# Kernel tuning notes

Hardware: AMD Instinct MI355X
Metric: run time of the kernel (lower is better)

The kernel has to match this reference:

```python
import jax, jax.numpy as jnp
import numpy as np

# ---- static config ----
B, H, W, C = 32, 64, 64, 256
WS, SHIFT, NH = 8, 4, 8
HD = C // NH
N = WS * WS  # tokens per window
NW = (H // WS) * (W // WS)
EPS = 1e-5


def _relative_position_index(ws):
    ch, cw = np.meshgrid(np.arange(ws), np.arange(ws), indexing='ij')
    coords = np.stack([ch, cw]).reshape(2, -1)          # (2, N)
    rel = coords[:, :, None] - coords[:, None, :]        # (2, N, N)
    rel = rel.transpose(1, 2, 0)
    rel[:, :, 0] += ws - 1
    rel[:, :, 1] += ws - 1
    rel[:, :, 0] *= 2 * ws - 1
    return jnp.asarray(rel.sum(-1))                      # (N, N) int


def _shifted_window_mask(h, w, ws, shift):
    img = np.zeros((h, w))
    slices = (slice(0, -ws), slice(-ws, -shift), slice(-shift, None))
    cnt = 0
    for hs in slices:
        for wsl in slices:
            img[hs, wsl] = cnt
            cnt += 1
    mw = img.reshape(h // ws, ws, w // ws, ws).transpose(0, 2, 1, 3).reshape(-1, ws * ws)
    diff = mw[:, None, :] - mw[:, :, None]
    return jnp.asarray(np.where(diff != 0, -100.0, 0.0).astype(np.float32))  # (nW, N, N)


REL_IDX = _relative_position_index(WS)
ATTN_MASK = _shifted_window_mask(H, W, WS, SHIFT)


def _layernorm(x, g, b):
    mu = jnp.mean(x, axis=-1, keepdims=True)
    var = jnp.mean(jnp.square(x - mu), axis=-1, keepdims=True)
    return (x - mu) * jax.lax.rsqrt(var + EPS) * g + b


def _window_partition(x):  # (B,H,W,C) -> (B*nW, N, C)
    x = x.reshape(B, H // WS, WS, W // WS, WS, C)
    return x.transpose(0, 1, 3, 2, 4, 5).reshape(-1, N, C)


def _window_reverse(win):  # (B*nW, N, C) -> (B,H,W,C)
    x = win.reshape(B, H // WS, W // WS, WS, WS, C)
    return x.transpose(0, 1, 3, 2, 4, 5).reshape(B, H, W, C)


def setup_inputs() -> dict:
    key = jax.random.key(0)
    ks = jax.random.split(key, 6)
    s = lambda fan_in: 1.0 / np.sqrt(fan_in)
    return {
        'x': jax.random.normal(ks[0], (B, H * W, C), jnp.float32),
        'norm1_g': jnp.ones((C,), jnp.float32),
        'norm1_b': jnp.zeros((C,), jnp.float32),
        'qkv_w': jax.random.normal(ks[1], (C, 3 * C), jnp.float32) * s(C),
        'qkv_b': jnp.zeros((3 * C,), jnp.float32),
        'proj_w': jax.random.normal(ks[2], (C, C), jnp.float32) * s(C),
        'proj_b': jnp.zeros((C,), jnp.float32),
        'bias_table': jax.random.normal(ks[3], ((2 * WS - 1) ** 2, NH), jnp.float32) * 0.02,
        'norm2_g': jnp.ones((C,), jnp.float32),
        'norm2_b': jnp.zeros((C,), jnp.float32),
        'fc1_w': jax.random.normal(ks[4], (C, 4 * C), jnp.float32) * s(C),
        'fc1_b': jnp.zeros((4 * C,), jnp.float32),
        'fc2_w': jax.random.normal(ks[5], (4 * C, C), jnp.float32) * s(4 * C),
        'fc2_b': jnp.zeros((C,), jnp.float32),
    }


def reference(x, norm1_g, norm1_b, qkv_w, qkv_b, proj_w, proj_b, bias_table,
              norm2_g, norm2_b, fc1_w, fc1_b, fc2_w, fc2_b):
    shortcut = x
    h = _layernorm(x, norm1_g, norm1_b).reshape(B, H, W, C)
    # cyclic shift
    h = jnp.roll(h, shift=(-SHIFT, -SHIFT), axis=(1, 2))
    xw = _window_partition(h)                               # (Bw, N, C), Bw = B*nW
    # window attention
    qkv = xw @ qkv_w + qkv_b                                 # (Bw, N, 3C)
    qkv = qkv.reshape(-1, N, 3, NH, HD).transpose(2, 0, 3, 1, 4)
    q, k, v = qkv[0], qkv[1], qkv[2]                         # (Bw, NH, N, HD)
    attn = jnp.einsum('whnd,whmd->whnm', q * (HD ** -0.5), k)
    rpb = bias_table[REL_IDX.reshape(-1)].reshape(N, N, NH).transpose(2, 0, 1)
    attn = attn + rpb[None]
    attn = attn.reshape(B, NW, NH, N, N) + ATTN_MASK[None, :, None]
    attn = jax.nn.softmax(attn.reshape(-1, NH, N, N), axis=-1)
    out = jnp.einsum('whnm,whmd->whnd', attn, v)
    out = out.transpose(0, 2, 1, 3).reshape(-1, N, C)
    out = out @ proj_w + proj_b
    # reverse windows + shift back
    h = _window_reverse(out)
    h = jnp.roll(h, shift=(SHIFT, SHIFT), axis=(1, 2)).reshape(B, H * W, C)
    x = shortcut + h
    # MLP with pre-norm residual
    m = _layernorm(x, norm2_g, norm2_b)
    m = jax.nn.gelu(m @ fc1_w + fc1_b, approximate=False) @ fc2_w + fc2_b
    return x + m
```

## Files before the change

### kernel.cpp

```cpp
#include <hip/hip_runtime.h>
#include <hip/hip_bf16.h>


typedef __bf16 bf16;
typedef __bf16 bf16x8 __attribute__((ext_vector_type(8)));
typedef __bf16 bf16x4 __attribute__((ext_vector_type(4)));
typedef float  f32x4  __attribute__((ext_vector_type(4)));

#define M_TOK 131072

#define GLDS(gp, lp)                                                                   \
    __builtin_amdgcn_global_load_lds(                                                  \
        (const __attribute__((address_space(1))) unsigned int*)(gp),                   \
        (__attribute__((address_space(3))) unsigned int*)(lp), 16, 0, 0)

__global__ __launch_bounds__(256) void prep_all(const float* __restrict__ qkv_w,
                                                const float* __restrict__ proj_w,
                                                const float* __restrict__ fc1_w,
                                                const float* __restrict__ fc2_w,
                                                const float* __restrict__ bt,
                                                bf16* __restrict__ WQ, bf16* __restrict__ WP,
                                                bf16* __restrict__ W1, bf16* __restrict__ W2,
                                                float* __restrict__ rpb) {
    int idx = blockIdx.x * 256 + threadIdx.x;
    if (idx < 196608) {
        int k = idx / 768, n = idx - k * 768;
        WQ[(size_t)n * 256 + k] = (bf16)qkv_w[idx];
    } else if (idx < 262144) {
        int l = idx - 196608;
        int k = l >> 8, n = l & 255;
        WP[(size_t)n * 256 + k] = (bf16)proj_w[l];
    } else if (idx < 524288) {
        int l = idx - 262144;
        int k = l >> 10, n = l & 1023;
        W1[(size_t)n * 256 + k] = (bf16)fc1_w[l];
    } else if (idx < 786432) {
        int l = idx - 524288;
        int k = l >> 8, n = l & 255;
        W2[(size_t)n * 1024 + k] = (bf16)fc2_w[l];
    } else {
        int l = idx - 786432;
        int h = l >> 12, n = (l >> 6) & 63, m = l & 63;
        int ridx = ((n >> 3) - (m >> 3) + 7) * 15 + ((n & 7) - (m & 7) + 7);
        rpb[l] = bt[ridx * 8 + h];
    }
}

__global__ __launch_bounds__(256) void ln_k(const float* __restrict__ x,
                                            const float* __restrict__ g,
                                            const float* __restrict__ bb,
                                            bf16* __restrict__ dst) {
    int t = blockIdx.x * 4 + (threadIdx.x >> 6);
    int lane = threadIdx.x & 63;
    int w = t >> 6, n = t & 63;
    int b = w >> 6, nw = w & 63;
    int r = ((nw >> 3) * 8 + (n >> 3) + 4) & 63;
    int c = ((nw & 7) * 8 + (n & 7) + 4) & 63;
    size_t src = ((size_t)b * 4096 + r * 64 + c) * 256;
    float4 v = *(const float4*)&x[src + lane * 4];
    float s = v.x + v.y + v.z + v.w;
    float sq = v.x * v.x + v.y * v.y + v.z * v.z + v.w * v.w;
#pragma unroll
    for (int off = 1; off < 64; off <<= 1) {
        s += __shfl_xor(s, off);
        sq += __shfl_xor(sq, off);
    }
    float mean = s * (1.0f / 256.0f);
    float var = sq * (1.0f / 256.0f) - mean * mean;
    float rstd = rsqrtf(var + 1e-5f);
    float4 gg = *(const float4*)&g[lane * 4];
    float4 bv = *(const float4*)&bb[lane * 4];
    bf16x4 o;
    o[0] = (bf16)((v.x - mean) * rstd * gg.x + bv.x);
    o[1] = (bf16)((v.y - mean) * rstd * gg.y + bv.y);
    o[2] = (bf16)((v.z - mean) * rstd * gg.z + bv.z);
    o[3] = (bf16)((v.w - mean) * rstd * gg.w + bv.w);
    *(bf16x4*)&dst[(size_t)t * 256 + lane * 4] = o;
}

__device__ __forceinline__ float fast_gelu(float v) {
    float t = v * v;
    float w = __builtin_fmaf(0.044715f * t, v, v);
    float e = __expf(-1.5957691216057308f * w);
    return v * __builtin_amdgcn_rcpf(1.0f + e);
}

template <int NDIM, int KDIM, int EPI>
__global__ __launch_bounds__(256) void gemm_k(const bf16* __restrict__ A,
                                              const bf16* __restrict__ Bt,
                                              const float* __restrict__ bias,
                                              bf16* __restrict__ outb,
                                              float* __restrict__ outf,
                                              const bf16* __restrict__ baseb) {
    __shared__ __align__(16) bf16 SH[24576];
    constexpr int NBN = NDIM / 128;
    constexpr int NK = KDIM / 32;
    const int tid = threadIdx.x;
    const int nwg = gridDim.x;
    const int flat = blockIdx.x;
    const int cpx = nwg >> 3;
    const int orig = (flat & 7) * cpx + (flat >> 3);
    const int bm = orig / NBN, bn = orig % NBN;

    const int lane = tid & 63, wid = tid >> 6;
    const int wr = wid >> 1, wc = wid & 1;
    const int lhi = lane >> 4, llo = lane & 15;

    f32x4 acc[4][4];
#pragma unroll
    for (int i = 0; i < 4; i++)
#pragma unroll
        for (int j = 0; j < 4; j++) acc[i][j] = f32x4{0.f, 0.f, 0.f, 0.f};

    const int srow = wid * 32 + (lane >> 2);
    const int scol = (((lane & 3) - ((lane >> 3) & 3)) & 3) * 8;
    const bf16* Ap = A + (size_t)(bm * 128 + srow) * KDIM + scol;
    const bf16* Bp = Bt + (size_t)(bn * 128 + srow) * KDIM + scol;
    const int gsw = ((lhi + (llo >> 1)) & 3) * 8;

#define STAGE(bufidx)                                                                  \
    do {                                                                               \
        bf16* Al = SH + (bufidx)*4096 + wid * 1024;                                    \
        bf16* Bl = SH + 12288 + (bufidx)*4096 + wid * 1024;                            \
        GLDS(Ap, Al);                                                                  \
        GLDS(Ap + 16 * KDIM, Al + 16 * 32);                                            \
        GLDS(Bp, Bl);                                                                  \
        GLDS(Bp + 16 * KDIM, Bl + 16 * 32);                                            \
        Ap += 32;                                                                      \
        Bp += 32;                                                                      \
    } while (0)

#define COMPUTE(bufidx)                                                                \
    do {                                                                               \
        const int ab = (bufidx)*4096;                                                  \
        bf16x8 af[4], bfr[4];                                                          \
        _Pragma("unroll") for (int mi = 0; mi < 4; mi++) af[mi] =                      \
            *(const bf16x8*)&SH[ab + (wr * 64 + mi * 16 + llo) * 32 + gsw];            \
        _Pragma("unroll") for (int ni = 0; ni < 4; ni++) bfr[ni] =                     \
            *(const bf16x8*)&SH[12288 + ab + (wc * 64 + ni * 16 + llo) * 32 + gsw];    \
        _Pragma("unroll") for (int mi = 0; mi < 4; mi++)                               \
            _Pragma("unroll") for (int ni = 0; ni < 4; ni++) acc[mi][ni] =             \
                __builtin_amdgcn_mfma_f32_16x16x32_bf16(bfr[ni], af[mi],               \
                                                        acc[mi][ni], 0, 0, 0);         \
    } while (0)

#define WAITBAR(N)                                                                     \
    asm volatile("s_waitcnt vmcnt(" #N ")" ::: "memory");                              \
    __builtin_amdgcn_s_barrier();                                                      \
    __builtin_amdgcn_sched_barrier(0)

#define END_PHASE                                                                      \
    asm volatile("s_waitcnt lgkmcnt(0)" ::: "memory");                                 \
    __builtin_amdgcn_s_barrier();                                                      \
    __builtin_amdgcn_sched_barrier(0)

    STAGE(0);
    STAGE(1);
    STAGE(2);
    int buf = 0;
    for (int i = 0; i + 3 < NK; ++i) {
        WAITBAR(8);
        COMPUTE(buf);
        END_PHASE;
        STAGE(buf);
        buf = (buf == 2) ? 0 : buf + 1;
    }
    WAITBAR(8);
    COMPUTE(buf);
    buf = (buf == 2) ? 0 : buf + 1;
    WAITBAR(4);
    COMPUTE(buf);
    buf = (buf == 2) ? 0 : buf + 1;
    WAITBAR(0);
    COMPUTE(buf);

#undef STAGE
#undef COMPUTE
#undef WAITBAR
#undef END_PHASE

    __syncthreads();

    char* shb = (char*)SH;
    if constexpr (EPI == 0 || EPI == 2) {
#pragma unroll
        for (int ni = 0; ni < 4; ni++) {
            const int lcol = wc * 64 + ni * 16 + lhi * 4;
            const float4 b4 = *(const float4*)&bias[bn * 128 + lcol];
#pragma unroll
            for (int mi = 0; mi < 4; mi++) {
                const int ltok = wr * 64 + mi * 16 + llo;
                float v0 = acc[mi][ni][0] + b4.x;
                float v1 = acc[mi][ni][1] + b4.y;
                float v2 = acc[mi][ni][2] + b4.z;
                float v3 = acc[mi][ni][3] + b4.w;
                bf16x4 o;
                if constexpr (EPI == 2) {
                    o[0] = (bf16)fast_gelu(v0); o[1] = (bf16)fast_gelu(v1);
                    o[2] = (bf16)fast_gelu(v2); o[3] = (bf16)fast_gelu(v3);
                } else {
                    o[0] = (bf16)v0; o[1] = (bf16)v1; o[2] = (bf16)v2; o[3] = (bf16)v3;
                }
                const int u2 = (lcol >> 3) ^ (ltok & 15);
                *(bf16x4*)(shb + ltok * 256 + u2 * 16 + (lcol & 7) * 2) = o;
            }
        }
        __syncthreads();
        const int j = lane & 15;
#pragma unroll
        for (int rnd = 0; rnd < 8; rnd++) {
            const int ltok = wid * 32 + rnd * 4 + (lane >> 4);
            const int u2 = j ^ (ltok & 15);
            bf16x8 v = *(const bf16x8*)(shb + ltok * 256 + u2 * 16);
            *(bf16x8*)&outb[(size_t)(bm * 128 + ltok) * NDIM + bn * 128 + j * 8] = v;
        }
    } else {
#pragma unroll
        for (int p = 0; p < 2; p++) {
            if (wc == p) {
#pragma unroll
                for (int ni = 0; ni < 4; ni++) {
                    const int lcolh = ni * 16 + lhi * 4;
                    const float4 b4 = *(const float4*)&bias[bn * 128 + p * 64 + lcolh];
#pragma unroll
                    for (int mi = 0; mi < 4; mi++) {
                        const int ltok = wr * 64 + mi * 16 + llo;
                        float4 o = {acc[mi][ni][0] + b4.x, acc[mi][ni][1] + b4.y,
                                    acc[mi][ni][2] + b4.z, acc[mi][ni][3] + b4.w};
                        const int u2 = (lcolh >> 2) ^ (ltok & 15);
                        *(float4*)(shb + ltok * 256 + u2 * 16) = o;
                    }
                }
            }
            __syncthreads();
            const int j = lane & 15;
#pragma unroll
            for (int rnd = 0; rnd < 8; rnd++) {
                const int ltok = wid * 32 + rnd * 4 + (lane >> 4);
                const int u2 = j ^ (ltok & 15);
                float4 v = *(const float4*)(shb + ltok * 256 + u2 * 16);
                const int gcol = bn * 128 + p * 64 + j * 4;
                const int grow = bm * 128 + ltok;
                size_t dst = (size_t)grow * NDIM + gcol;
                bf16x4 bb = *(const bf16x4*)&baseb[dst];
                float4 o = {v.x + (float)bb[0], v.y + (float)bb[1],
                            v.z + (float)bb[2], v.w + (float)bb[3]};
                *(float4*)&outf[dst] = o;
            }
            if (p == 0) __syncthreads();
        }
    }
}

__global__ __launch_bounds__(256) void proj_ln_k(const bf16* __restrict__ A,
                                                 const bf16* __restrict__ Bt,
                                                 const float* __restrict__ bias,
                                                 const float* __restrict__ resid,
                                                 bf16* __restrict__ baseb,
                                                 const float* __restrict__ g2,
                                                 const float* __restrict__ b2,
                                                 bf16* __restrict__ hb) {
    __shared__ __align__(16) bf16 SH[20480];
    constexpr int KDIM = 256;
    const int tid = threadIdx.x;
    const int nwg = gridDim.x;
    const int flat = blockIdx.x;
    const int cpx = nwg >> 3;
    const int bm = (flat & 7) * cpx + (flat >> 3);

    const int lane = tid & 63, wid = tid >> 6;
    const int lhi = lane >> 4, llo = lane & 15;

    f32x4 acc[4][4];
#pragma unroll
    for (int i = 0; i < 4; i++)
#pragma unroll
        for (int j = 0; j < 4; j++) acc[i][j] = f32x4{0.f, 0.f, 0.f, 0.f};

    const int scol = (((lane & 3) - ((lane >> 3) & 3)) & 3) * 8;
    const bf16* Ap = A + (size_t)(bm * 64 + wid * 16 + (lane >> 2)) * KDIM + scol;
    const bf16* Bp = Bt + (size_t)(wid * 64 + (lane >> 2)) * KDIM + scol;
    const int gsw = ((lhi + (llo >> 1)) & 3) * 8;

#define PSTAGE(bufidx)                                                                 \
    do {                                                                               \
        bf16* Al = SH + (bufidx)*2048 + wid * 512;                                     \
        bf16* Bl = SH + 4096 + (bufidx)*8192 + wid * 2048;                             \
        GLDS(Ap, Al);                                                                  \
        GLDS(Bp, Bl);                                                                  \
        GLDS(Bp + 16 * KDIM, Bl + 512);                                                \
        GLDS(Bp + 32 * KDIM, Bl + 1024);                                               \
        GLDS(Bp + 48 * KDIM, Bl + 1536);                                               \
        Ap += 32;                                                                      \
        Bp += 32;                                                                      \
    } while (0)

#define PCOMPUTE(bufidx)                                                               \
    do {                                                                               \
        bf16x8 af[4], bfr[4];                                                          \
        _Pragma("unroll") for (int mi = 0; mi < 4; mi++) af[mi] =                      \
            *(const bf16x8*)&SH[(bufidx)*2048 + (mi * 16 + llo) * 32 + gsw];           \
        _Pragma("unroll") for (int ni = 0; ni < 4; ni++) bfr[ni] =                     \
            *(const bf16x8*)&SH[4096 + (bufidx)*8192 +                                 \
                                (wid * 64 + ni * 16 + llo) * 32 + gsw];                \
        _Pragma("unroll") for (int mi = 0; mi < 4; mi++)                               \
            _Pragma("unroll") for (int ni = 0; ni < 4; ni++) acc[mi][ni] =             \
                __builtin_amdgcn_mfma_f32_16x16x32_bf16(bfr[ni], af[mi],               \
                                                        acc[mi][ni], 0, 0, 0);         \
    } while (0)

    PSTAGE(0);
    PSTAGE(1);
    int buf = 0;
    for (int i = 0; i + 2 < 8; ++i) {
        asm volatile("s_waitcnt vmcnt(5)" ::: "memory");
        __builtin_amdgcn_s_barrier();
        __builtin_amdgcn_sched_barrier(0);
        PCOMPUTE(buf);
        asm volatile("s_waitcnt lgkmcnt(0)" ::: "memory");
        __builtin_amdgcn_s_barrier();
        __builtin_amdgcn_sched_barrier(0);
        PSTAGE(buf);
        buf ^= 1;
    }
    asm volatile("s_waitcnt vmcnt(5)" ::: "memory");
    __builtin_amdgcn_s_barrier();
    __builtin_amdgcn_sched_barrier(0);
    PCOMPUTE(buf);
    buf ^= 1;
    asm volatile("s_waitcnt vmcnt(0)" ::: "memory");
    __builtin_amdgcn_s_barrier();
    __builtin_amdgcn_sched_barrier(0);
    PCOMPUTE(buf);

#undef PSTAGE
#undef PCOMPUTE

    char* shb = (char*)SH;
    const float4 gg = *(const float4*)&g2[lane * 4];
    const float4 bb4 = *(const float4*)&b2[lane * 4];
#pragma unroll
    for (int p = 0; p < 2; p++) {
        __syncthreads();
#pragma unroll
        for (int ni = 0; ni < 4; ni++) {
            const int col0 = wid * 64 + ni * 16 + lhi * 4;
            const float4 b4 = *(const float4*)&bias[col0];
#pragma unroll
            for (int m2 = 0; m2 < 2; m2++) {
                const int mi = 2 * p + m2;
                const int lt = m2 * 16 + llo;
                float4 o = {acc[mi][ni][0] + b4.x, acc[mi][ni][1] + b4.y,
                            acc[mi][ni][2] + b4.z, acc[mi][ni][3] + b4.w};
                const int u2 = (col0 >> 2) ^ (lt & 15);
                *(float4*)(shb + lt * 1024 + u2 * 16) = o;
            }
        }
        __syncthreads();
#pragma unroll
        for (int rnd = 0; rnd < 8; rnd++) {
            const int lt = rnd * 4 + wid;
            const int u2 = lane ^ (lt & 15);
            float4 v = *(const float4*)(shb + lt * 1024 + u2 * 16);
            const int grow = bm * 64 + p * 32 + lt;
            int w = grow >> 6, n = grow & 63;
            int b = w >> 6, nw = w & 63;
            int rr = ((nw >> 3) * 8 + (n >> 3) + 4) & 63;
            int cc = ((nw & 7) * 8 + (n & 7) + 4) & 63;
            const size_t rowbase = ((size_t)b * 4096 + rr * 64 + cc) * 256;
            float4 rs = *(const float4*)&resid[rowbase + lane * 4];
            float4 o = {rs.x + v.x, rs.y + v.y, rs.z + v.z, rs.w + v.w};
            bf16x4 bo = {(bf16)o.x, (bf16)o.y, (bf16)o.z, (bf16)o.w};
            *(bf16x4*)&baseb[rowbase + lane * 4] = bo;
            float s = o.x + o.y + o.z + o.w;
            float sq = o.x * o.x + o.y * o.y + o.z * o.z + o.w * o.w;
#pragma unroll
            for (int off = 1; off < 64; off <<= 1) {
                s += __shfl_xor(s, off);
                sq += __shfl_xor(sq, off);
            }
            float mean = s * (1.0f / 256.0f);
            float var = sq * (1.0f / 256.0f) - mean * mean;
            float rstd = rsqrtf(var + 1e-5f);
            bf16x4 ho;
            ho[0] = (bf16)((o.x - mean) * rstd * gg.x + bb4.x);
            ho[1] = (bf16)((o.y - mean) * rstd * gg.y + bb4.y);
            ho[2] = (bf16)((o.z - mean) * rstd * gg.z + bb4.z);
            ho[3] = (bf16)((o.w - mean) * rstd * gg.w + bb4.w);
            *(bf16x4*)&hb[rowbase + lane * 4] = ho;
        }
    }
}

__device__ __forceinline__ int regid3(int p) { return p < 56 ? 0 : (p < 60 ? 1 : 2); }

__global__ __launch_bounds__(256) void attn_k(const bf16* __restrict__ qkv,
                                              const float* __restrict__ rpb,
                                              bf16* __restrict__ aout) {
    __shared__ __align__(16) bf16 Pl[4][64 * 80];
    const int wid = threadIdx.x >> 6, lane = threadIdx.x & 63;
    const int lhi = lane >> 4, llo = lane & 15;
    const int wh = blockIdx.x * 4 + wid;
    const int w = wh >> 3, h = wh & 7;
    const bf16* base = qkv + (size_t)w * (64 * 768);

    bf16x8 qf[4], kf[4];
#pragma unroll
    for (int i = 0; i < 4; i++)
        qf[i] = *(const bf16x8*)(base + (i * 16 + llo) * 768 + h * 32 + lhi * 8);
#pragma unroll
    for (int i = 0; i < 4; i++)
        kf[i] = *(const bf16x8*)(base + (i * 16 + llo) * 768 + 256 + h * 32 + lhi * 8);
    f32x4 s[4][4];
#pragma unroll
    for (int mi = 0; mi < 4; mi++)
#pragma unroll
        for (int ni = 0; ni < 4; ni++) {
            s[mi][ni] = f32x4{0.f, 0.f, 0.f, 0.f};
            s[mi][ni] =
                __builtin_amdgcn_mfma_f32_16x16x32_bf16(qf[mi], kf[ni], s[mi][ni], 0, 0, 0);
        }

    const int nw = w & 63;
    const int pr0 = (nw >> 3) * 8, pc0 = (nw & 7) * 8;
    int creg[4];
#pragma unroll
    for (int ni = 0; ni < 4; ni++) {
        int m = ni * 16 + llo;
        creg[ni] = regid3(pr0 + (m >> 3)) * 3 + regid3(pc0 + (m & 7));
    }
    float rmax[4][4], rsum[4][4];
#pragma unroll
    for (int mi = 0; mi < 4; mi++)
#pragma unroll
        for (int r = 0; r < 4; r++) {
            int n = mi * 16 + lhi * 4 + r;
            int rreg = regid3(pr0 + (n >> 3)) * 3 + regid3(pc0 + (n & 7));
            float mx = -1e30f;
#pragma unroll
            for (int ni = 0; ni < 4; ni++) {
                int m = ni * 16 + llo;
                float sv = s[mi][ni][r] * 0.17677669529663687f + rpb[(h * 64 + n) * 64 + m] +
                           (rreg == creg[ni] ? 0.0f : -100.0f);
                s[mi][ni][r] = sv;
                mx = fmaxf(mx, sv);
            }
            rmax[mi][r] = mx;
        }
#pragma unroll
    for (int off = 1; off < 16; off <<= 1)
#pragma unroll
        for (int mi = 0; mi < 4; mi++)
#pragma unroll
            for (int r = 0; r < 4; r++)
                rmax[mi][r] = fmaxf(rmax[mi][r], __shfl_xor(rmax[mi][r], off));
#pragma unroll
    for (int mi = 0; mi < 4; mi++)
#pragma unroll
        for (int r = 0; r < 4; r++) {
            float a = 0.f;
#pragma unroll
            for (int ni = 0; ni < 4; ni++) {
                float p = __expf(s[mi][ni][r] - rmax[mi][r]);
                s[mi][ni][r] = p;
                a += p;
            }
            rsum[mi][r] = a;
        }
#pragma unroll
    for (int off = 1; off < 16; off <<= 1)
#pragma unroll
        for (int mi = 0; mi < 4; mi++)
#pragma unroll
            for (int r = 0; r < 4; r++) rsum[mi][r] += __shfl_xor(rsum[mi][r], off);

    bf16* P = Pl[wid];
#pragma unroll
    for (int mi = 0; mi < 4; mi++)
#pragma unroll
        for (int r = 0; r < 4; r++) {
            float rinv = 1.0f / rsum[mi][r];
            int row = mi * 16 + lhi * 4 + r;
#pragma unroll
            for (int ni = 0; ni < 4; ni++)
                P[row * 80 + ni * 16 + llo] = (bf16)(s[mi][ni][r] * rinv);
        }

    f32x4 o[4][2];
#pragma unroll
    for (int mi = 0; mi < 4; mi++)
#pragma unroll
        for (int ni = 0; ni < 2; ni++) o[mi][ni] = f32x4{0.f, 0.f, 0.f, 0.f};
#pragma unroll
    for (int kc = 0; kc < 2; kc++) {
        bf16x8 pf[4], vf[2];
#pragma unroll
        for (int mi = 0; mi < 4; mi++)
            pf[mi] = *(const bf16x8*)(P + (mi * 16 + llo) * 80 + kc * 32 + lhi * 8);
#pragma unroll
        for (int ni = 0; ni < 2; ni++)
#pragma unroll
            for (int j = 0; j < 8; j++)
                vf[ni][j] = base[(kc * 32 + lhi * 8 + j) * 768 + 512 + h * 32 + ni * 16 + llo];
#pragma unroll
        for (int mi = 0; mi < 4; mi++)
#pragma unroll
            for (int ni = 0; ni < 2; ni++)
                o[mi][ni] =
                    __builtin_amdgcn_mfma_f32_16x16x32_bf16(pf[mi], vf[ni], o[mi][ni], 0, 0, 0);
    }
#pragma unroll
    for (int mi = 0; mi < 4; mi++)
#pragma unroll
        for (int ni = 0; ni < 2; ni++)
#pragma unroll
            for (int r = 0; r < 4; r++) {
                int row = mi * 16 + lhi * 4 + r;
                aout[(size_t)(w * 64 + row) * 256 + h * 32 + ni * 16 + llo] =
                    (bf16)o[mi][ni][r];
            }
}

extern "C" void kernel_launch(void* const* d_in, const int* in_sizes, int n_in,
                              void* d_out, int out_size, void* d_ws, size_t ws_size,
                              hipStream_t stream) {
    const float* x      = (const float*)d_in[0];
    const float* n1g    = (const float*)d_in[1];
    const float* n1b    = (const float*)d_in[2];
    const float* qkv_w  = (const float*)d_in[3];
    const float* qkv_b  = (const float*)d_in[4];
    const float* proj_w = (const float*)d_in[5];
    const float* proj_b = (const float*)d_in[6];
    const float* btab   = (const float*)d_in[7];
    const float* n2g    = (const float*)d_in[8];
    const float* n2b    = (const float*)d_in[9];
    const float* fc1_w  = (const float*)d_in[10];
    const float* fc1_b  = (const float*)d_in[11];
    const float* fc2_w  = (const float*)d_in[12];
    const float* fc2_b  = (const float*)d_in[13];
    float* out = (float*)d_out;
    char* ws = (char*)d_ws;

    constexpr size_t MB = 1048576ull;
    bf16* XW    = (bf16*)(ws);
    bf16* BASEB = (bf16*)(ws);
    bf16* QKVB  = (bf16*)(ws + 67 * MB);
    bf16* Gbuf  = (bf16*)(ws + 67 * MB);
    bf16* Hb    = (bf16*)(ws + 201 * MB);
    bf16* ATTN  = (bf16*)(ws + 268 * MB);
    bf16* WQ    = (bf16*)(ws + 335 * MB);
    bf16* WP    = (bf16*)(ws + 335 * MB + 393216);
    bf16* W1    = (bf16*)(ws + 335 * MB + 524288);
    bf16* W2    = (bf16*)(ws + 335 * MB + 1048576);
    float* RPB  = (float*)(ws + 335 * MB + 1572864);

    dim3 blk(256);
    prep_all<<<3200, blk, 0, stream>>>(qkv_w, proj_w, fc1_w, fc2_w, btab,
                                       WQ, WP, W1, W2, RPB);

    ln_k<<<M_TOK / 4, blk, 0, stream>>>(x, n1g, n1b, XW);

    for (int c = 0; c < 2; ++c) {
        const size_t toff = (size_t)c * 65536;
        gemm_k<768, 256, 0><<<3072, blk, 0, stream>>>(XW + toff * 256, WQ, qkv_b,
                                                      QKVB, nullptr, nullptr);
        attn_k<<<2048, blk, 0, stream>>>(QKVB, RPB, ATTN + toff * 256);
    }

    proj_ln_k<<<2048, blk, 0, stream>>>(ATTN, WP, proj_b, x, BASEB, n2g, n2b, Hb);

    for (int q = 0; q < 2; ++q) {
        const size_t toff = (size_t)q * 65536;
        gemm_k<1024, 256, 2><<<4096, blk, 0, stream>>>(Hb + toff * 256, W1, fc1_b,
                                                       Gbuf, nullptr, nullptr);
        gemm_k<256, 1024, 3><<<1024, blk, 0, stream>>>(Gbuf, W2, fc2_b, nullptr,
                                                       out + toff * 256,
                                                       BASEB + toff * 256);
    }
}
```

Measured before the change: 584.4 us.

## Chunk whole block into four token slices and triple-buffer proj GEMM

```diff
diff --git a/kernel.cpp b/kernel.cpp
--- a/kernel.cpp
+++ b/kernel.cpp
@@ -6,8 +6,6 @@
 typedef __bf16 bf16x8 __attribute__((ext_vector_type(8)));
 typedef __bf16 bf16x4 __attribute__((ext_vector_type(4)));
 typedef float  f32x4  __attribute__((ext_vector_type(4)));
-
-#define M_TOK 131072
 
 #define GLDS(gp, lp)                                                                   \
     __builtin_amdgcn_global_load_lds(                                                  \
@@ -260,7 +258,7 @@
                                                  const float* __restrict__ g2,
                                                  const float* __restrict__ b2,
                                                  bf16* __restrict__ hb) {
-    __shared__ __align__(16) bf16 SH[20480];
+    __shared__ __align__(16) bf16 SH[32768];
     constexpr int KDIM = 256;
     const int tid = threadIdx.x;
     const int nwg = gridDim.x;
@@ -285,7 +283,7 @@
 #define PSTAGE(bufidx)                                                                 \
     do {                                                                               \
         bf16* Al = SH + (bufidx)*2048 + wid * 512;                                     \
-        bf16* Bl = SH + 4096 + (bufidx)*8192 + wid * 2048;                             \
+        bf16* Bl = SH + 6144 + (bufidx)*8192 + wid * 2048;                             \
         GLDS(Ap, Al);                                                                  \
         GLDS(Bp, Bl);                                                                  \
         GLDS(Bp + 16 * KDIM, Bl + 512);                                                \
@@ -301,7 +299,7 @@
         _Pragma("unroll") for (int mi = 0; mi < 4; mi++) af[mi] =                      \
             *(const bf16x8*)&SH[(bufidx)*2048 + (mi * 16 + llo) * 32 + gsw];           \
         _Pragma("unroll") for (int ni = 0; ni < 4; ni++) bfr[ni] =                     \
-            *(const bf16x8*)&SH[4096 + (bufidx)*8192 +                                 \
+            *(const bf16x8*)&SH[6144 + (bufidx)*8192 +                                 \
                                 (wid * 64 + ni * 16 + llo) * 32 + gsw];                \
         _Pragma("unroll") for (int mi = 0; mi < 4; mi++)                               \
             _Pragma("unroll") for (int ni = 0; ni < 4; ni++) acc[mi][ni] =             \
@@ -309,86 +307,88 @@
                                                         acc[mi][ni], 0, 0, 0);         \
     } while (0)
 
+#define PWAITBAR(N)                                                                    \
+    asm volatile("s_waitcnt vmcnt(" #N ")" ::: "memory");                              \
+    __builtin_amdgcn_s_barrier();                                                      \
+    __builtin_amdgcn_sched_barrier(0)
+
     PSTAGE(0);
     PSTAGE(1);
+    PSTAGE(2);
     int buf = 0;
-    for (int i = 0; i + 2 < 8; ++i) {
-        asm volatile("s_waitcnt vmcnt(5)" ::: "memory");
-        __builtin_amdgcn_s_barrier();
-        __builtin_amdgcn_sched_barrier(0);
+    for (int i = 0; i + 3 < 8; ++i) {
+        PWAITBAR(10);
         PCOMPUTE(buf);
         asm volatile("s_waitcnt lgkmcnt(0)" ::: "memory");
         __builtin_amdgcn_s_barrier();
         __builtin_amdgcn_sched_barrier(0);
         PSTAGE(buf);
-        buf ^= 1;
-    }
-    asm volatile("s_waitcnt vmcnt(5)" ::: "memory");
-    __builtin_amdgcn_s_barrier();
-    __builtin_amdgcn_sched_barrier(0);
+        buf = (buf == 2) ? 0 : buf + 1;
+    }
+    PWAITBAR(10);
     PCOMPUTE(buf);
-    buf ^= 1;
-    asm volatile("s_waitcnt vmcnt(0)" ::: "memory");
-    __builtin_amdgcn_s_barrier();
-    __builtin_amdgcn_sched_barrier(0);
+    buf = (buf == 2) ? 0 : buf + 1;
+    PWAITBAR(5);
+    PCOMPUTE(buf);
+    buf = (buf == 2) ? 0 : buf + 1;
+    PWAITBAR(0);
     PCOMPUTE(buf);
 
 #undef PSTAGE
 #undef PCOMPUTE
+#undef PWAITBAR
+
+    __syncthreads();
 
     char* shb = (char*)SH;
+#pragma unroll
+    for (int ni = 0; ni < 4; ni++) {
+        const int col0 = wid * 64 + ni * 16 + lhi * 4;
+        const float4 b4 = *(const float4*)&bias[col0];
+#pragma unroll
+        for (int mi = 0; mi < 4; mi++) {
+            const int ltok = mi * 16 + llo;
+            float4 o = {acc[mi][ni][0] + b4.x, acc[mi][ni][1] + b4.y,
+                        acc[mi][ni][2] + b4.z, acc[mi][ni][3] + b4.w};
+            const int u2 = (col0 >> 2) ^ (ltok & 15);
+            *(float4*)(shb + ltok * 1024 + u2 * 16) = o;
+        }
+    }
+    __syncthreads();
+
     const float4 gg = *(const float4*)&g2[lane * 4];
     const float4 bb4 = *(const float4*)&b2[lane * 4];
 #pragma unroll
-    for (int p = 0; p < 2; p++) {
-        __syncthreads();
-#pragma unroll
-        for (int ni = 0; ni < 4; ni++) {
-            const int col0 = wid * 64 + ni * 16 + lhi * 4;
-            const float4 b4 = *(const float4*)&bias[col0];
-#pragma unroll
-            for (int m2 = 0; m2 < 2; m2++) {
-                const int mi = 2 * p + m2;
-                const int lt = m2 * 16 + llo;
-                float4 o = {acc[mi][ni][0] + b4.x, acc[mi][ni][1] + b4.y,
-                            acc[mi][ni][2] + b4.z, acc[mi][ni][3] + b4.w};
-                const int u2 = (col0 >> 2) ^ (lt & 15);
-                *(float4*)(shb + lt * 1024 + u2 * 16) = o;
-            }
-        }
-        __syncthreads();
-#pragma unroll
-        for (int rnd = 0; rnd < 8; rnd++) {
-            const int lt = rnd * 4 + wid;
-            const int u2 = lane ^ (lt & 15);
-            float4 v = *(const float4*)(shb + lt * 1024 + u2 * 16);
-            const int grow = bm * 64 + p * 32 + lt;
-            int w = grow >> 6, n = grow & 63;
-            int b = w >> 6, nw = w & 63;
-            int rr = ((nw >> 3) * 8 + (n >> 3) + 4) & 63;
-            int cc = ((nw & 7) * 8 + (n & 7) + 4) & 63;
-            const size_t rowbase = ((size_t)b * 4096 + rr * 64 + cc) * 256;
-            float4 rs = *(const float4*)&resid[rowbase + lane * 4];
-            float4 o = {rs.x + v.x, rs.y + v.y, rs.z + v.z, rs.w + v.w};
-            bf16x4 bo = {(bf16)o.x, (bf16)o.y, (bf16)o.z, (bf16)o.w};
-            *(bf16x4*)&baseb[rowbase + lane * 4] = bo;
-            float s = o.x + o.y + o.z + o.w;
-            float sq = o.x * o.x + o.y * o.y + o.z * o.z + o.w * o.w;
-#pragma unroll
-            for (int off = 1; off < 64; off <<= 1) {
-                s += __shfl_xor(s, off);
-                sq += __shfl_xor(sq, off);
-            }
-            float mean = s * (1.0f / 256.0f);
-            float var = sq * (1.0f / 256.0f) - mean * mean;
-            float rstd = rsqrtf(var + 1e-5f);
-            bf16x4 ho;
-            ho[0] = (bf16)((o.x - mean) * rstd * gg.x + bb4.x);
-            ho[1] = (bf16)((o.y - mean) * rstd * gg.y + bb4.y);
-            ho[2] = (bf16)((o.z - mean) * rstd * gg.z + bb4.z);
-            ho[3] = (bf16)((o.w - mean) * rstd * gg.w + bb4.w);
-            *(bf16x4*)&hb[rowbase + lane * 4] = ho;
-        }
+    for (int rnd = 0; rnd < 16; rnd++) {
+        const int t = rnd * 4 + wid;
+        const int u2 = lane ^ (t & 15);
+        float4 v = *(const float4*)(shb + t * 1024 + u2 * 16);
+        const int grow = bm * 64 + t;
+        int w = grow >> 6, n = grow & 63;
+        int b = w >> 6, nw = w & 63;
+        int rr = ((nw >> 3) * 8 + (n >> 3) + 4) & 63;
+        int cc = ((nw & 7) * 8 + (n & 7) + 4) & 63;
+        const size_t rowbase = ((size_t)b * 4096 + rr * 64 + cc) * 256;
+        float4 rs = *(const float4*)&resid[rowbase + lane * 4];
+        float4 o = {rs.x + v.x, rs.y + v.y, rs.z + v.z, rs.w + v.w};
+        bf16x4 bo = {(bf16)o.x, (bf16)o.y, (bf16)o.z, (bf16)o.w};
+        *(bf16x4*)&baseb[rowbase + lane * 4] = bo;
+        float s = o.x + o.y + o.z + o.w;
+        float sq = o.x * o.x + o.y * o.y + o.z * o.z + o.w * o.w;
+#pragma unroll
+        for (int off = 1; off < 64; off <<= 1) {
+            s += __shfl_xor(s, off);
+            sq += __shfl_xor(sq, off);
+        }
+        float mean = s * (1.0f / 256.0f);
+        float var = sq * (1.0f / 256.0f) - mean * mean;
+        float rstd = rsqrtf(var + 1e-5f);
+        bf16x4 ho;
+        ho[0] = (bf16)((o.x - mean) * rstd * gg.x + bb4.x);
+        ho[1] = (bf16)((o.y - mean) * rstd * gg.y + bb4.y);
+        ho[2] = (bf16)((o.z - mean) * rstd * gg.z + bb4.z);
+        ho[3] = (bf16)((o.w - mean) * rstd * gg.w + bb4.w);
+        *(bf16x4*)&hb[rowbase + lane * 4] = ho;
     }
 }
 
@@ -542,39 +542,33 @@
     char* ws = (char*)d_ws;
 
     constexpr size_t MB = 1048576ull;
-    bf16* XW    = (bf16*)(ws);
-    bf16* BASEB = (bf16*)(ws);
-    bf16* QKVB  = (bf16*)(ws + 67 * MB);
-    bf16* Gbuf  = (bf16*)(ws + 67 * MB);
-    bf16* Hb    = (bf16*)(ws + 201 * MB);
-    bf16* ATTN  = (bf16*)(ws + 268 * MB);
-    bf16* WQ    = (bf16*)(ws + 335 * MB);
-    bf16* WP    = (bf16*)(ws + 335 * MB + 393216);
-    bf16* W1    = (bf16*)(ws + 335 * MB + 524288);
-    bf16* W2    = (bf16*)(ws + 335 * MB + 1048576);
-    float* RPB  = (float*)(ws + 335 * MB + 1572864);
+    bf16* XWc   = (bf16*)(ws);
+    bf16* QKVc  = (bf16*)(ws + 17 * MB);
+    bf16* ATTNc = (bf16*)(ws + 68 * MB);
+    bf16* BASEc = (bf16*)(ws + 85 * MB);
+    bf16* Hbc   = (bf16*)(ws + 102 * MB);
+    bf16* Gc    = (bf16*)(ws + 119 * MB);
+    bf16* WQ    = (bf16*)(ws + 187 * MB);
+    bf16* WP    = (bf16*)(ws + 187 * MB + 393216);
+    bf16* W1    = (bf16*)(ws + 187 * MB + 524288);
+    bf16* W2    = (bf16*)(ws + 187 * MB + 1048576);
+    float* RPB  = (float*)(ws + 187 * MB + 1572864);
 
     dim3 blk(256);
     prep_all<<<3200, blk, 0, stream>>>(qkv_w, proj_w, fc1_w, fc2_w, btab,
                                        WQ, WP, W1, W2, RPB);
 
-    ln_k<<<M_TOK / 4, blk, 0, stream>>>(x, n1g, n1b, XW);
-
-    for (int c = 0; c < 2; ++c) {
-        const size_t toff = (size_t)c * 65536;
-        gemm_k<768, 256, 0><<<3072, blk, 0, stream>>>(XW + toff * 256, WQ, qkv_b,
-                                                      QKVB, nullptr, nullptr);
-        attn_k<<<2048, blk, 0, stream>>>(QKVB, RPB, ATTN + toff * 256);
-    }
-
-    proj_ln_k<<<2048, blk, 0, stream>>>(ATTN, WP, proj_b, x, BASEB, n2g, n2b, Hb);
-
-    for (int q = 0; q < 2; ++q) {
-        const size_t toff = (size_t)q * 65536;
-        gemm_k<1024, 256, 2><<<4096, blk, 0, stream>>>(Hb + toff * 256, W1, fc1_b,
-                                                       Gbuf, nullptr, nullptr);
-        gemm_k<256, 1024, 3><<<1024, blk, 0, stream>>>(Gbuf, W2, fc2_b, nullptr,
-                                                       out + toff * 256,
-                                                       BASEB + toff * 256);
-    }
-}
+    for (int c = 0; c < 4; ++c) {
+        const size_t xo = (size_t)c * 32768 * 256;
+        ln_k<<<8192, blk, 0, stream>>>(x + xo, n1g, n1b, XWc);
+        gemm_k<768, 256, 0><<<1536, blk, 0, stream>>>(XWc, WQ, qkv_b, QKVc,
+                                                      nullptr, nullptr);
+        attn_k<<<1024, blk, 0, stream>>>(QKVc, RPB, ATTNc);
+        proj_ln_k<<<512, blk, 0, stream>>>(ATTNc, WP, proj_b, x + xo, BASEc,
+                                           n2g, n2b, Hbc);
+        gemm_k<1024, 256, 2><<<2048, blk, 0, stream>>>(Hbc, W1, fc1_b, Gc,
+                                                       nullptr, nullptr);
+        gemm_k<256, 1024, 3><<<512, blk, 0, stream>>>(Gc, W2, fc2_b, nullptr,
+                                                      out + xo, BASEc);
+    }
+}
```

Measured after the change: 532.7 us. 1.1x faster.
